# Kernel tuning notes

Measured on AMD Instinct MI355X. Metric: run time of the kernel, lower is better.

Reference implementation:

```python
import jax, jax.numpy as jnp
import numpy as np

B, S, D, H = 2, 2048, 4096, 16
HD = D // H          # 256 head dim
ROT = 64             # rotary_dim
MASK_FILL = -65504.0 # fp16 min, as in the IPEX kernel


def _sinusoidal_positions(num_pos, dim):
    inv_freq = 1.0 / (10000.0 ** (np.arange(0, dim, 2, dtype=np.float32) / dim))
    sinusoid = np.einsum('i,j->ij', np.arange(num_pos, dtype=np.float32), inv_freq)
    return np.concatenate([np.sin(sinusoid), np.cos(sinusoid)], axis=-1).astype(np.float32)  # [num_pos, dim]


def setup_inputs() -> dict:
    key = jax.random.key(0)
    ks = jax.random.split(key, 6)
    w = 0.02
    return {
        'hidden_states': jax.random.normal(ks[0], (B, S, D), jnp.float32),
        'Wq': jax.random.normal(ks[1], (D, D), jnp.float32) * w,
        'Wk': jax.random.normal(ks[2], (D, D), jnp.float32) * w,
        'Wv': jax.random.normal(ks[3], (D, D), jnp.float32) * w,
        'Wo': jax.random.normal(ks[4], (D, D), jnp.float32) * w,
        'embed_positions': jnp.asarray(_sinusoidal_positions(S, ROT)),  # [max_pos, ROT] sin|cos
        'attention_mask': jnp.zeros((B, 1, 1, S), jnp.float32),
        'position_ids': jnp.tile(jnp.arange(S, dtype=jnp.int32), (B, 1)),
    }


def rotate_every_two(x):
    x1 = x[..., ::2]
    x2 = x[..., 1::2]
    return jnp.stack((-x2, x1), axis=-1).reshape(x.shape)


def reference(hidden_states, Wq, Wk, Wv, Wo, embed_positions, attention_mask, position_ids):
    b, s, d = hidden_states.shape
    q = (hidden_states @ Wq).reshape(b, s, H, HD)
    k = (hidden_states @ Wk).reshape(b, s, H, HD)
    v = (hidden_states @ Wv).reshape(b, s, H, HD)

    # gather sin/cos per position, GPT-J interleaved layout
    sincos = embed_positions[position_ids]            # [b, s, ROT]
    sin, cos = jnp.split(sincos, 2, axis=-1)          # each [b, s, ROT/2]
    sin = jnp.repeat(sin, 2, axis=-1)[:, :, None, :]  # [b, s, 1, ROT]
    cos = jnp.repeat(cos, 2, axis=-1)[:, :, None, :]

    def rope(t):
        tr = t[..., :ROT]
        tr = tr * cos + rotate_every_two(tr) * sin
        return jnp.concatenate([tr, t[..., ROT:]], axis=-1)

    q = rope(q).transpose(0, 2, 1, 3)  # [b, H, s, HD]
    k = rope(k).transpose(0, 2, 1, 3)
    v = v.transpose(0, 2, 1, 3)

    scores = jnp.einsum('bhqd,bhkd->bhqk', q, k)
    causal = jnp.tril(jnp.ones((s, s), bool))
    # IPEX order: mask-fill with -65504 BEFORE dividing by sqrt(head_dim)
    scores = jnp.where(causal, scores, MASK_FILL) / jnp.sqrt(jnp.float32(HD))
    scores = scores + attention_mask
    attn = jax.nn.softmax(scores, axis=-1)

    out = jnp.einsum('bhqk,bhkd->bhqd', attn, v)
    out = out.transpose(0, 2, 1, 3).reshape(b, s, d)
    return out @ Wo
```

## Files before the change

kernel.cpp:

```cpp
#include <hip/hip_runtime.h>

typedef __bf16 bf16x8 __attribute__((ext_vector_type(8)));
typedef float f32x4 __attribute__((ext_vector_type(4)));
typedef unsigned short u16;
typedef unsigned int u32;
typedef u16 u16x8 __attribute__((ext_vector_type(8)));
typedef u16 u16x4 __attribute__((ext_vector_type(4)));

#define DEVI __device__ __forceinline__

static constexpr size_t R_ELEMS = (size_t)4096 * 4096;

DEVI u16 f2bf(float f) {
  u32 x = __float_as_uint(f);
  u32 r = x + 0x7FFFu + ((x >> 16) & 1u);
  return (u16)(r >> 16);
}
DEVI float bf2f(u16 u) { return __uint_as_float(((u32)u) << 16); }

#define GLOAD_LDS16(gp, lp)                                                     \
  __builtin_amdgcn_global_load_lds(                                             \
      (const __attribute__((address_space(1))) void*)(gp),                      \
      (__attribute__((address_space(3))) void*)(lp), 16, 0, 0)

#define MFMA16(a, b, c) __builtin_amdgcn_mfma_f32_16x16x32_bf16((a), (b), (c), 0, 0, 0)

__global__ void k_cvt(const float* __restrict__ in, u16* __restrict__ out, int n8) {
  int i = blockIdx.x * blockDim.x + threadIdx.x;
  if (i >= n8) return;
  const float4* p = (const float4*)in + (size_t)i * 2;
  float4 a = p[0], b = p[1];
  u16x8 o;
  o[0] = f2bf(a.x); o[1] = f2bf(a.y); o[2] = f2bf(a.z); o[3] = f2bf(a.w);
  o[4] = f2bf(b.x); o[5] = f2bf(b.y); o[6] = f2bf(b.z); o[7] = f2bf(b.w);
  *((u16x8*)out + i) = o;
}

__global__ void k_transpose_w(const float* __restrict__ W, u16* __restrict__ Wt) {
  __shared__ float t[64][65];
  int kb = blockIdx.x * 64, nb = blockIdx.y * 64;
  int tx = threadIdx.x, ty = threadIdx.y;
#pragma unroll
  for (int i = 0; i < 16; i++) {
    int r = i * 4 + ty;
    t[r][tx] = W[(size_t)(kb + r) * 4096 + nb + tx];
  }
  __syncthreads();
#pragma unroll
  for (int i = 0; i < 16; i++) {
    int r = i * 4 + ty;
    Wt[(size_t)(nb + r) * 4096 + kb + tx] = f2bf(t[tx][r]);
  }
}

__global__ void k_transpose_v(const u16* __restrict__ V, u16* __restrict__ Vt) {
  __shared__ u16 t[64][65];
  int s0 = blockIdx.x * 64, d0 = blockIdx.y * 64;
  size_t base = (size_t)blockIdx.z * (2048 * 256);
  int tx = threadIdx.x, ty = threadIdx.y;
#pragma unroll
  for (int i = 0; i < 16; i++) {
    int r = i * 4 + ty;
    t[r][tx] = V[base + (size_t)(s0 + r) * 256 + d0 + tx];
  }
  __syncthreads();
#pragma unroll
  for (int i = 0; i < 16; i++) {
    int r = i * 4 + ty;
    Vt[base + (size_t)(d0 + r) * 2048 + s0 + tx] = t[tx][r];
  }
}

__global__ void k_rope(u16* __restrict__ q, u16* __restrict__ k,
                       const float* __restrict__ ep, const int* __restrict__ pid) {
  int gid = blockIdx.x * blockDim.x + threadIdx.x;
  int pair = gid & 31;
  int row = gid >> 5;
  u16* base = (row < 65536) ? q : k;
  int rr = row & 65535;
  int b = rr >> 15;
  int s = rr & 2047;
  int pos = pid[b * 2048 + s];
  float sn = ep[pos * 64 + pair];
  float cs = ep[pos * 64 + 32 + pair];
  u16* p = base + (size_t)rr * 256 + pair * 2;
  float x0 = bf2f(p[0]), x1 = bf2f(p[1]);
  p[0] = f2bf(x0 * cs - x1 * sn);
  p[1] = f2bf(x1 * cs + x0 * sn);
}

template <int OUTMODE>
__global__ __launch_bounds__(256, 2) void k_gemm(const u16* __restrict__ A,
                                                 const u16* __restrict__ Bt,
                                                 void* __restrict__ outp) {
  __shared__ __attribute__((aligned(16))) u16 lA[128 * 64];
  __shared__ __attribute__((aligned(16))) u16 lB[128 * 64];
  const int tid = threadIdx.x;
  const int w = tid >> 6, lane = tid & 63;
  const int wr = w >> 1, wc = w & 1;
  const int m0 = blockIdx.y * 128, n0 = blockIdx.x * 128;

  f32x4 acc[4][4];
#pragma unroll
  for (int i = 0; i < 4; i++)
#pragma unroll
    for (int j = 0; j < 4; j++) acc[i][j] = (f32x4){0.f, 0.f, 0.f, 0.f};

  const int srow = lane >> 3;
  const int scol = ((lane & 7) ^ srow) * 8;
  const u16* Abase = A + (size_t)(m0 + w * 32 + srow) * 4096 + scol;
  const u16* Bbase = Bt + (size_t)(n0 + w * 32 + srow) * 4096 + scol;
  u16* lAw = lA + w * 2048;
  u16* lBw = lB + w * 2048;

  const int lm = lane & 15;
  const int lk = lane >> 4;
  const int swz = (lane & 7) << 3;

  for (int kt = 0; kt < 64; ++kt) {
    __syncthreads();
#pragma unroll
    for (int i = 0; i < 4; ++i) {
      GLOAD_LDS16(Abase + (size_t)kt * 64 + (size_t)i * 8 * 4096, lAw + i * 512);
      GLOAD_LDS16(Bbase + (size_t)kt * 64 + (size_t)i * 8 * 4096, lBw + i * 512);
    }
    __syncthreads();
#pragma unroll
    for (int ks = 0; ks < 2; ++ks) {
      bf16x8 af[4], bfr[4];
      const int ce = (ks * 32 + lk * 8) ^ swz;
#pragma unroll
      for (int mi = 0; mi < 4; mi++)
        af[mi] = *(const bf16x8*)(lA + (wr * 64 + mi * 16 + lm) * 64 + ce);
#pragma unroll
      for (int ni = 0; ni < 4; ni++)
        bfr[ni] = *(const bf16x8*)(lB + (wc * 64 + ni * 16 + lm) * 64 + ce);
#pragma unroll
      for (int mi = 0; mi < 4; mi++)
#pragma unroll
        for (int ni = 0; ni < 4; ni++)
          acc[mi][ni] = MFMA16(af[mi], bfr[ni], acc[mi][ni]);
    }
  }

#pragma unroll
  for (int mi = 0; mi < 4; mi++) {
#pragma unroll
    for (int ni = 0; ni < 4; ni++) {
#pragma unroll
      for (int r = 0; r < 4; r++) {
        int m = m0 + wr * 64 + mi * 16 + lk * 4 + r;
        int n = n0 + wc * 64 + ni * 16 + lm;
        float v = acc[mi][ni][r];
        if (OUTMODE == 0) {
          u16* o = (u16*)outp;
          o[(size_t)((m >> 11) * 16 + (n >> 8)) * 524288 + (size_t)(m & 2047) * 256 +
            (n & 255)] = f2bf(v);
        } else {
          float* o = (float*)outp;
          o[(size_t)m * 4096 + n] = v;
        }
      }
    }
  }
}

__global__ __launch_bounds__(256, 2) void k_gemm_qk(const u16* __restrict__ A,
                                                    const u16* __restrict__ Btq,
                                                    const u16* __restrict__ Btk,
                                                    u16* __restrict__ Qo,
                                                    u16* __restrict__ Ko) {
  __shared__ __attribute__((aligned(16))) u16 lA[128 * 64];
  __shared__ __attribute__((aligned(16))) u16 lBq[128 * 64];
  __shared__ __attribute__((aligned(16))) u16 lBk[128 * 64];
  const int tid = threadIdx.x;
  const int w = tid >> 6, lane = tid & 63;
  const int wr = w >> 1, wc = w & 1;
  const int m0 = blockIdx.y * 128, n0 = blockIdx.x * 128;

  f32x4 accq[4][4], acck[4][4];
#pragma unroll
  for (int i = 0; i < 4; i++)
#pragma unroll
    for (int j = 0; j < 4; j++) {
      accq[i][j] = (f32x4){0.f, 0.f, 0.f, 0.f};
      acck[i][j] = (f32x4){0.f, 0.f, 0.f, 0.f};
    }

  const int srow = lane >> 3;
  const int scol = ((lane & 7) ^ srow) * 8;
  const u16* Abase = A + (size_t)(m0 + w * 32 + srow) * 4096 + scol;
  const u16* Bqb = Btq + (size_t)(n0 + w * 32 + srow) * 4096 + scol;
  const u16* Bkb = Btk + (size_t)(n0 + w * 32 + srow) * 4096 + scol;
  u16* lAw = lA + w * 2048;
  u16* lBqw = lBq + w * 2048;
  u16* lBkw = lBk + w * 2048;

  const int lm = lane & 15;
  const int lk = lane >> 4;
  const int swz = (lane & 7) << 3;

  for (int kt = 0; kt < 64; ++kt) {
    __syncthreads();
#pragma unroll
    for (int i = 0; i < 4; ++i) {
      GLOAD_LDS16(Abase + (size_t)kt * 64 + (size_t)i * 8 * 4096, lAw + i * 512);
      GLOAD_LDS16(Bqb + (size_t)kt * 64 + (size_t)i * 8 * 4096, lBqw + i * 512);
      GLOAD_LDS16(Bkb + (size_t)kt * 64 + (size_t)i * 8 * 4096, lBkw + i * 512);
    }
    __syncthreads();
#pragma unroll
    for (int ks = 0; ks < 2; ++ks) {
      bf16x8 af[4], bfr[4];
      const int ce = (ks * 32 + lk * 8) ^ swz;
#pragma unroll
      for (int mi = 0; mi < 4; mi++)
        af[mi] = *(const bf16x8*)(lA + (wr * 64 + mi * 16 + lm) * 64 + ce);
#pragma unroll
      for (int ni = 0; ni < 4; ni++)
        bfr[ni] = *(const bf16x8*)(lBq + (wc * 64 + ni * 16 + lm) * 64 + ce);
#pragma unroll
      for (int mi = 0; mi < 4; mi++)
#pragma unroll
        for (int ni = 0; ni < 4; ni++)
          accq[mi][ni] = MFMA16(af[mi], bfr[ni], accq[mi][ni]);
#pragma unroll
      for (int ni = 0; ni < 4; ni++)
        bfr[ni] = *(const bf16x8*)(lBk + (wc * 64 + ni * 16 + lm) * 64 + ce);
#pragma unroll
      for (int mi = 0; mi < 4; mi++)
#pragma unroll
        for (int ni = 0; ni < 4; ni++)
          acck[mi][ni] = MFMA16(af[mi], bfr[ni], acck[mi][ni]);
    }
  }

#pragma unroll
  for (int mi = 0; mi < 4; mi++) {
#pragma unroll
    for (int ni = 0; ni < 4; ni++) {
#pragma unroll
      for (int r = 0; r < 4; r++) {
        int m = m0 + wr * 64 + mi * 16 + lk * 4 + r;
        int n = n0 + wc * 64 + ni * 16 + lm;
        size_t idx = (size_t)((m >> 11) * 16 + (n >> 8)) * 524288 +
                     (size_t)(m & 2047) * 256 + (n & 255);
        Qo[idx] = f2bf(accq[mi][ni][r]);
        Ko[idx] = f2bf(acck[mi][ni][r]);
      }
    }
  }
}

__global__ __launch_bounds__(512, 2) void k_attn(const u16* __restrict__ Q,
                                                 const u16* __restrict__ K,
                                                 const u16* __restrict__ Vt,
                                                 const float* __restrict__ amask,
                                                 u16* __restrict__ AO) {
  __shared__ __attribute__((aligned(16))) u16 lK[2][64 * 256];
  __shared__ __attribute__((aligned(16))) u16 lV[2][256 * 64];
  __shared__ __attribute__((aligned(16))) u16 lP[8][16 * 64];

  const int tid = threadIdx.x, w = tid >> 6, lane = tid & 63;
  const int wg = blockIdx.x;
  const int bh = wg & 31;
  const int qt = (wg < 256) ? (15 - (wg >> 5)) : ((wg - 256) >> 5);
  const int b = bh >> 4;
  const int lm = lane & 15, lk = lane >> 4;
  const size_t head = (size_t)bh * (2048 * 256);
  const int q0 = qt * 128 + w * 16;
  const int swzl = (lane & 7) << 3;

  const int kreg_row = (lane >> 5);
  const int kcol = (lane & 31) * 8;
  const int vreg_row = (lane >> 3);
  const int vcol = (lane & 7) * 8;

#define ASTAGE(t)                                                                \
  {                                                                              \
    const int bb_ = (t) & 1;                                                     \
    const int kv0_ = (t) * 64;                                                   \
    _Pragma("unroll") for (int i_ = 0; i_ < 4; i_++) {                           \
      const int reg_ = w + i_ * 8;                                               \
      const int krow_ = reg_ * 2 + kreg_row;                                     \
      GLOAD_LDS16(K + head + (size_t)(kv0_ + krow_) * 256 +                      \
                      (kcol ^ ((krow_ & 7) << 3)),                               \
                  &lK[bb_][reg_ * 512 + lane * 8]);                              \
      const int vrow_ = reg_ * 8 + vreg_row;                                     \
      GLOAD_LDS16(Vt + head + (size_t)vrow_ * 2048 + kv0_ +                      \
                      (vcol ^ ((vrow_ & 7) << 3)),                               \
                  &lV[bb_][reg_ * 512 + lane * 8]);                              \
    }                                                                            \
  }

  bf16x8 qf[8];
#pragma unroll
  for (int c = 0; c < 8; c++)
    qf[c] = *(const bf16x8*)(Q + head + (size_t)(q0 + lm) * 256 + c * 32 + lk * 8);

  f32x4 o[16];
#pragma unroll
  for (int i = 0; i < 16; i++) o[i] = (f32x4){0.f, 0.f, 0.f, 0.f};
  float m_s = -__builtin_inff();
  float l_s = 0.f;

  const int ntiles = 2 * qt + 2;
  ASTAGE(0);

  for (int t = 0; t < ntiles; ++t) {
    const int kv0 = t * 64;
    const int bb = t & 1;
    float4 amq[4];
#pragma unroll
    for (int kb = 0; kb < 4; kb++)
      amq[kb] = *(const float4*)(amask + b * 2048 + kv0 + kb * 16 + lk * 4);
    if (t + 1 < ntiles) {
      ASTAGE(t + 1);
      asm volatile("s_waitcnt vmcnt(8)" ::: "memory");
    } else {
      asm volatile("s_waitcnt vmcnt(0)" ::: "memory");
    }
    __builtin_amdgcn_s_barrier();

    if (q0 + 15 >= kv0) {
      const u16* lKb = lK[bb];
      const u16* lVb = lV[bb];

      float sx[4][4];
      __builtin_amdgcn_s_setprio(1);
#pragma unroll
      for (int kb = 0; kb < 4; kb++) {
        f32x4 sa = (f32x4){0.f, 0.f, 0.f, 0.f};
        const int kvr = kb * 16 + lm;
#pragma unroll
        for (int c = 0; c < 8; c++) {
          bf16x8 kf = *(const bf16x8*)(lKb + kvr * 256 + ((c * 32 + lk * 8) ^ swzl));
          sa = __builtin_amdgcn_mfma_f32_16x16x32_bf16(kf, qf[c], sa, 0, 0, 0);
        }
#pragma unroll
        for (int r = 0; r < 4; r++)
          sx[kb][r] = sa[r] * 0.0625f + ((const float*)&amq[kb])[r];
      }
      __builtin_amdgcn_s_setprio(0);

      const int q_abs = q0 + lm;
      float tm = -__builtin_inff();
#pragma unroll
      for (int kb = 0; kb < 4; kb++)
#pragma unroll
        for (int r = 0; r < 4; r++) {
          bool valid = (kv0 + kb * 16 + lk * 4 + r) <= q_abs;
          tm = fmaxf(tm, valid ? sx[kb][r] : -__builtin_inff());
        }
      tm = fmaxf(tm, __shfl_xor(tm, 16, 64));
      tm = fmaxf(tm, __shfl_xor(tm, 32, 64));

      if (!__all(tm <= m_s + 8.0f)) {
        float mnew = fmaxf(m_s, tm);
        float alpha = __expf(m_s - mnew);
        m_s = mnew;
        l_s *= alpha;
        float af0 = __shfl(alpha, lk * 4 + 0, 64);
        float af1 = __shfl(alpha, lk * 4 + 1, 64);
        float af2 = __shfl(alpha, lk * 4 + 2, 64);
        float af3 = __shfl(alpha, lk * 4 + 3, 64);
#pragma unroll
        for (int dblk = 0; dblk < 16; dblk++) {
          o[dblk][0] *= af0; o[dblk][1] *= af1;
          o[dblk][2] *= af2; o[dblk][3] *= af3;
        }
      }

      float psum = 0.f;
#pragma unroll
      for (int kb = 0; kb < 4; kb++) {
        u16x4 ph;
#pragma unroll
        for (int r = 0; r < 4; r++) {
          bool valid = (kv0 + kb * 16 + lk * 4 + r) <= q_abs;
          float p = valid ? __expf(sx[kb][r] - m_s) : 0.f;
          psum += p;
          ph[r] = f2bf(p);
        }
        *(u16x4*)(&lP[w][lm * 64 + ((kb * 16 + lk * 4) ^ swzl)]) = ph;
      }
      psum += __shfl_xor(psum, 16, 64);
      psum += __shfl_xor(psum, 32, 64);
      l_s += psum;

      bf16x8 pa[2];
#pragma unroll
      for (int kh = 0; kh < 2; kh++)
        pa[kh] = *(const bf16x8*)(&lP[w][lm * 64 + ((lk * 8 + kh * 32) ^ swzl)]);
      __builtin_amdgcn_s_setprio(1);
#pragma unroll
      for (int dblk = 0; dblk < 16; dblk++) {
        const int dr = dblk * 16 + lm;
#pragma unroll
        for (int kh = 0; kh < 2; kh++) {
          bf16x8 vf = *(const bf16x8*)(lVb + dr * 64 + ((lk * 8 + kh * 32) ^ swzl));
          o[dblk] = __builtin_amdgcn_mfma_f32_16x16x32_bf16(pa[kh], vf, o[dblk], 0, 0, 0);
        }
      }
      __builtin_amdgcn_s_setprio(0);
    }
    __builtin_amdgcn_s_barrier();
  }
#undef ASTAGE

  float linv[4];
#pragma unroll
  for (int r = 0; r < 4; r++) linv[r] = 1.0f / __shfl(l_s, lk * 4 + r, 64);
#pragma unroll
  for (int r = 0; r < 4; r++) {
    const int s_abs = q0 + lk * 4 + r;
#pragma unroll
    for (int dblk = 0; dblk < 16; dblk++) {
      int d = (bh & 15) * 256 + dblk * 16 + lm;
      AO[((size_t)b * 2048 + s_abs) * 4096 + d] = f2bf(o[dblk][r] * linv[r]);
    }
  }
}

extern "C" void kernel_launch(void* const* d_in, const int* in_sizes, int n_in,
                              void* d_out, int out_size, void* d_ws, size_t ws_size,
                              hipStream_t stream) {
  (void)in_sizes; (void)n_in; (void)out_size; (void)ws_size;
  const float* hs = (const float*)d_in[0];
  const float* Wq = (const float*)d_in[1];
  const float* Wk = (const float*)d_in[2];
  const float* Wv = (const float*)d_in[3];
  const float* Wo = (const float*)d_in[4];
  const float* ep = (const float*)d_in[5];
  const float* am = (const float*)d_in[6];
  const int* pid = (const int*)d_in[7];

  u16* r0 = (u16*)d_ws;
  u16* r1 = r0 + R_ELEMS;
  u16* r2 = r1 + R_ELEMS;
  u16* r3 = r2 + R_ELEMS;
  u16* r4 = r3 + R_ELEMS;
  float* out = (float*)d_out;

  dim3 b256(256), b512(512), bT(64, 4);
  k_cvt<<<dim3(8192), b256, 0, stream>>>(hs, r0, 16777216 / 8);

  k_transpose_w<<<dim3(64, 64), bT, 0, stream>>>(Wq, r1);
  k_transpose_w<<<dim3(64, 64), bT, 0, stream>>>(Wk, r2);
  k_gemm_qk<<<dim3(32, 32), b256, 0, stream>>>(r0, r1, r2, r3, r4);

  k_transpose_w<<<dim3(64, 64), bT, 0, stream>>>(Wv, r1);
  k_gemm<0><<<dim3(32, 32), b256, 0, stream>>>(r0, r1, r2);

  k_rope<<<dim3(16384), b256, 0, stream>>>(r3, r4, ep, pid);
  k_transpose_v<<<dim3(32, 4, 32), bT, 0, stream>>>(r2, r0);

  k_attn<<<dim3(512), b512, 0, stream>>>(r3, r4, r0, am, r2);

  k_transpose_w<<<dim3(64, 64), bT, 0, stream>>>(Wo, r1);
  k_gemm<1><<<dim3(32, 32), b256, 0, stream>>>(r2, r1, out);
}
```

Measured before the change: 750.7 us.

## Fuse RoPE into QK GEMM epilogue and V transpose into V GEMM store

Applies rotary embedding to Q and K inside the QK projection epilogue, using lane shuffles to pair elements. The V projection now writes directly in transposed head layout with vectorized stores. This removes the separate rope and V-transpose kernels and their memory passes. Also remaps block ids to a 1D grid with a swizzled order, intended to improve cache reuse. It adds per-element sin/cos loads in the epilogue and strided transposed stores.

```diff
diff --git a/kernel.cpp b/kernel.cpp
--- a/kernel.cpp
+++ b/kernel.cpp
@@ -53,42 +53,6 @@
   }
 }
 
-__global__ void k_transpose_v(const u16* __restrict__ V, u16* __restrict__ Vt) {
-  __shared__ u16 t[64][65];
-  int s0 = blockIdx.x * 64, d0 = blockIdx.y * 64;
-  size_t base = (size_t)blockIdx.z * (2048 * 256);
-  int tx = threadIdx.x, ty = threadIdx.y;
-#pragma unroll
-  for (int i = 0; i < 16; i++) {
-    int r = i * 4 + ty;
-    t[r][tx] = V[base + (size_t)(s0 + r) * 256 + d0 + tx];
-  }
-  __syncthreads();
-#pragma unroll
-  for (int i = 0; i < 16; i++) {
-    int r = i * 4 + ty;
-    Vt[base + (size_t)(d0 + r) * 2048 + s0 + tx] = t[tx][r];
-  }
-}
-
-__global__ void k_rope(u16* __restrict__ q, u16* __restrict__ k,
-                       const float* __restrict__ ep, const int* __restrict__ pid) {
-  int gid = blockIdx.x * blockDim.x + threadIdx.x;
-  int pair = gid & 31;
-  int row = gid >> 5;
-  u16* base = (row < 65536) ? q : k;
-  int rr = row & 65535;
-  int b = rr >> 15;
-  int s = rr & 2047;
-  int pos = pid[b * 2048 + s];
-  float sn = ep[pos * 64 + pair];
-  float cs = ep[pos * 64 + 32 + pair];
-  u16* p = base + (size_t)rr * 256 + pair * 2;
-  float x0 = bf2f(p[0]), x1 = bf2f(p[1]);
-  p[0] = f2bf(x0 * cs - x1 * sn);
-  p[1] = f2bf(x1 * cs + x0 * sn);
-}
-
 template <int OUTMODE>
 __global__ __launch_bounds__(256, 2) void k_gemm(const u16* __restrict__ A,
                                                  const u16* __restrict__ Bt,
@@ -98,7 +62,9 @@
   const int tid = threadIdx.x;
   const int w = tid >> 6, lane = tid & 63;
   const int wr = w >> 1, wc = w & 1;
-  const int m0 = blockIdx.y * 128, n0 = blockIdx.x * 128;
+  const int bid = blockIdx.x;
+  const int wg = (bid & 7) * 128 + (bid >> 3);
+  const int m0 = (wg >> 5) * 128, n0 = (wg & 31) * 128;
 
   f32x4 acc[4][4];
 #pragma unroll
@@ -147,19 +113,19 @@
   for (int mi = 0; mi < 4; mi++) {
 #pragma unroll
     for (int ni = 0; ni < 4; ni++) {
-#pragma unroll
-      for (int r = 0; r < 4; r++) {
-        int m = m0 + wr * 64 + mi * 16 + lk * 4 + r;
-        int n = n0 + wc * 64 + ni * 16 + lm;
-        float v = acc[mi][ni][r];
-        if (OUTMODE == 0) {
-          u16* o = (u16*)outp;
-          o[(size_t)((m >> 11) * 16 + (n >> 8)) * 524288 + (size_t)(m & 2047) * 256 +
-            (n & 255)] = f2bf(v);
-        } else {
-          float* o = (float*)outp;
-          o[(size_t)m * 4096 + n] = v;
-        }
+      const int mb = m0 + wr * 64 + mi * 16 + lk * 4;
+      const int n = n0 + wc * 64 + ni * 16 + lm;
+      if (OUTMODE == 2) {
+        u16x4 vt;
+#pragma unroll
+        for (int r = 0; r < 4; r++) vt[r] = f2bf(acc[mi][ni][r]);
+        u16* o = (u16*)outp;
+        *(u16x4*)&o[(size_t)((mb >> 11) * 16 + ((n >> 8) & 15)) * 524288 +
+                    (size_t)(n & 255) * 2048 + (mb & 2047)] = vt;
+      } else {
+        float* o = (float*)outp;
+#pragma unroll
+        for (int r = 0; r < 4; r++) o[(size_t)(mb + r) * 4096 + n] = acc[mi][ni][r];
       }
     }
   }
@@ -168,6 +134,8 @@
 __global__ __launch_bounds__(256, 2) void k_gemm_qk(const u16* __restrict__ A,
                                                     const u16* __restrict__ Btq,
                                                     const u16* __restrict__ Btk,
+                                                    const float* __restrict__ ep,
+                                                    const int* __restrict__ pid,
                                                     u16* __restrict__ Qo,
                                                     u16* __restrict__ Ko) {
   __shared__ __attribute__((aligned(16))) u16 lA[128 * 64];
@@ -176,7 +144,9 @@
   const int tid = threadIdx.x;
   const int w = tid >> 6, lane = tid & 63;
   const int wr = w >> 1, wc = w & 1;
-  const int m0 = blockIdx.y * 128, n0 = blockIdx.x * 128;
+  const int bid = blockIdx.x;
+  const int wg = (bid & 7) * 128 + (bid >> 3);
+  const int m0 = (wg >> 5) * 128, n0 = (wg & 31) * 128;
 
   f32x4 accq[4][4], acck[4][4];
 #pragma unroll
@@ -235,6 +205,28 @@
     }
   }
 
+  const bool ropew = (((wg & 31) & 1) == 0) && (wc == 0);
+  if (ropew) {
+#pragma unroll
+    for (int mi = 0; mi < 4; mi++) {
+#pragma unroll
+      for (int r = 0; r < 4; r++) {
+        const int m = m0 + wr * 64 + mi * 16 + lk * 4 + r;
+        const int pos = pid[(m >> 11) * 2048 + (m & 2047)];
+#pragma unroll
+        for (int ni = 0; ni < 4; ni++) {
+          const int p = (ni * 16 + lm) >> 1;
+          const float sn = ep[pos * 64 + p];
+          const float cs = ep[pos * 64 + 32 + p];
+          float q = accq[mi][ni][r], k = acck[mi][ni][r];
+          float qp = __shfl_xor(q, 1, 64), kp = __shfl_xor(k, 1, 64);
+          accq[mi][ni][r] = (lm & 1) ? (q * cs + qp * sn) : (q * cs - qp * sn);
+          acck[mi][ni][r] = (lm & 1) ? (k * cs + kp * sn) : (k * cs - kp * sn);
+        }
+      }
+    }
+  }
+
 #pragma unroll
   for (int mi = 0; mi < 4; mi++) {
 #pragma unroll
@@ -243,7 +235,7 @@
       for (int r = 0; r < 4; r++) {
         int m = m0 + wr * 64 + mi * 16 + lk * 4 + r;
         int n = n0 + wc * 64 + ni * 16 + lm;
-        size_t idx = (size_t)((m >> 11) * 16 + (n >> 8)) * 524288 +
+        size_t idx = (size_t)((m >> 11) * 16 + ((n >> 8) & 15)) * 524288 +
                      (size_t)(m & 2047) * 256 + (n & 255);
         Qo[idx] = f2bf(accq[mi][ni][r]);
         Ko[idx] = f2bf(acck[mi][ni][r]);
@@ -447,16 +439,13 @@
 
   k_transpose_w<<<dim3(64, 64), bT, 0, stream>>>(Wq, r1);
   k_transpose_w<<<dim3(64, 64), bT, 0, stream>>>(Wk, r2);
-  k_gemm_qk<<<dim3(32, 32), b256, 0, stream>>>(r0, r1, r2, r3, r4);
+  k_gemm_qk<<<dim3(1024), b256, 0, stream>>>(r0, r1, r2, ep, pid, r3, r4);
 
   k_transpose_w<<<dim3(64, 64), bT, 0, stream>>>(Wv, r1);
-  k_gemm<0><<<dim3(32, 32), b256, 0, stream>>>(r0, r1, r2);
-
-  k_rope<<<dim3(16384), b256, 0, stream>>>(r3, r4, ep, pid);
-  k_transpose_v<<<dim3(32, 4, 32), bT, 0, stream>>>(r2, r0);
-
-  k_attn<<<dim3(512), b512, 0, stream>>>(r3, r4, r0, am, r2);
+  k_gemm<2><<<dim3(1024), b256, 0, stream>>>(r0, r1, r2);
+
+  k_attn<<<dim3(512), b512, 0, stream>>>(r3, r4, r2, am, r0);
 
   k_transpose_w<<<dim3(64, 64), bT, 0, stream>>>(Wo, r1);
-  k_gemm<1><<<dim3(32, 32), b256, 0, stream>>>(r2, r1, out);
-}
+  k_gemm<1><<<dim3(1024), b256, 0, stream>>>(r0, r1, out);
+}
```

New measurement: 789.9 us. +5.2%, slower.
